# Performance work log

Measured on AMD Instinct MI355X. Metric: run time of the kernel, lower is better.

Reference implementation:

```python
import jax, jax.numpy as jnp
import numpy as np

N, E, HID, NS, NC, NCLS, NG = 100000, 1200000, 64, 16, 8, 2, 512
EPS = 1e-5


def setup_inputs() -> dict:
    key = jax.random.key(0)
    ks = jax.random.split(key, 16)
    inp = {
        "shape_id": jax.random.randint(ks[0], (N,), 0, NS),
        "colour_id": jax.random.randint(ks[1], (N,), 0, NC),
        "edge_index": jax.random.randint(ks[2], (2, E), 0, N),
        "batch": jnp.sort(jax.random.randint(ks[3], (N,), 0, NG)),
        # embeddings
        "shape_W": jax.random.normal(ks[4], (NS, HID), jnp.float32) * 0.02,
        "col_W": jax.random.normal(ks[5], (NC, HID), jnp.float32) * 0.02,
        # SAGEConv 1: lin_l (on aggregated neighbors, with bias), lin_r (on self, no bias)
        "W1l": jax.random.normal(ks[6], (HID, HID), jnp.float32) * 0.05,
        "b1": jnp.zeros((HID,), jnp.float32),
        "W1r": jax.random.normal(ks[7], (HID, HID), jnp.float32) * 0.05,
        "g1": jnp.ones((HID,), jnp.float32),
        "be1": jnp.zeros((HID,), jnp.float32),
        # SAGEConv 2
        "W2l": jax.random.normal(ks[8], (HID, HID), jnp.float32) * 0.05,
        "b2": jnp.zeros((HID,), jnp.float32),
        "W2r": jax.random.normal(ks[9], (HID, HID), jnp.float32) * 0.05,
        "g2": jnp.ones((HID,), jnp.float32),
        "be2": jnp.zeros((HID,), jnp.float32),
        # classifier
        "Wlin": jax.random.normal(ks[10], (HID, NCLS), jnp.float32) * 0.05,
        "blin": jnp.zeros((NCLS,), jnp.float32),
    }
    return inp


def _sage(x, edge_index, Wl, bl, Wr):
    # PyG SAGEConv with mean aggregation: lin_l(mean_{j in N(i)} x_j) + lin_r(x_i)
    src, dst = edge_index[0], edge_index[1]
    n = x.shape[0]
    msg_sum = jax.ops.segment_sum(x[src], dst, num_segments=n)  # [N, HID]
    cnt = jax.ops.segment_sum(jnp.ones((src.shape[0],), x.dtype), dst, num_segments=n)
    mean = msg_sum / jnp.maximum(cnt, 1.0)[:, None]
    return mean @ Wl + bl + x @ Wr


def _bn(x, gamma, beta):
    # batch-statistics normalization over node dim (training-mode BatchNorm1d)
    mu = x.mean(0)
    var = x.var(0)
    return (x - mu) * jax.lax.rsqrt(var + EPS) * gamma + beta


def reference(shape_id, colour_id, edge_index, batch,
              shape_W, col_W, W1l, b1, W1r, g1, be1,
              W2l, b2, W2r, g2, be2, Wlin, blin):
    x = shape_W[shape_id] + col_W[colour_id]                  # [N, HID]
    x = jax.nn.relu(_bn(_sage(x, edge_index, W1l, b1, W1r), g1, be1))
    # dropout(0.3) treated as identity (eval mode)
    x = jax.nn.relu(_bn(_sage(x, edge_index, W2l, b2, W2r), g2, be2))
    graph_x = jax.ops.segment_sum(x, batch, num_segments=NG)  # global_add_pool
    return graph_x @ Wlin + blin                              # [NG, NCLS]
```

## Files before the change

kernel.cpp:

```cpp
#include <hip/hip_runtime.h>
#include <stdint.h>

#define N_NODES 100000
#define N_EDGES 1200000
#define HID 64
#define NGRAPH 512
#define NCLS 2
#define BN_EPS 1e-5f

#define NTILES (N_NODES / 16)
#define NBLK_G2 782

#define BKT_SH 10
#define BKT_NODES 1024
#define NB 98
#define BKT_CAP 16000
#define EB_PER_BLK 4096
#define NBLK_E 293

typedef __attribute__((ext_vector_type(8))) short short8;
typedef __attribute__((ext_vector_type(4))) float f32x4;

__device__ inline float bf2f(uint32_t hi16) {
    uint32_t u = hi16 << 16;
    return __builtin_bit_cast(float, u);
}
__device__ inline uint32_t f2bf_rtn(float f) {
    uint32_t u = __builtin_bit_cast(uint32_t, f);
    return (u + 0x7FFFu + ((u >> 16) & 1u)) >> 16;
}

__global__ void k_code(const int* __restrict__ sid, const int* __restrict__ cid,
                       unsigned char* __restrict__ code8) {
    int i = blockIdx.x * blockDim.x + threadIdx.x;
    if (i < N_NODES) code8[i] = (unsigned char)(sid[i] | (cid[i] << 4));
}

__global__ __launch_bounds__(256) void k_tab(const float* __restrict__ sW,
                                             const float* __restrict__ cW,
                                             const float* __restrict__ W1l,
                                             const float* __restrict__ W1r,
                                             const float* __restrict__ b1,
                                             float* __restrict__ TsL,
                                             ushort* __restrict__ tblR) {
    int gid = blockIdx.x * 256 + threadIdx.x;
    if (gid < 24 * 64) {
        int row = gid >> 6, d = gid & 63;
        const float* e = (row < 16) ? &sW[row * 64] : &cW[(row - 16) * 64];
        float acc = 0.f;
        #pragma unroll 8
        for (int k = 0; k < 64; ++k) acc += e[k] * W1l[k * 64 + d];
        TsL[gid] = acc;
    } else if (gid < 24 * 64 + 128 * 64) {
        int r = gid - 24 * 64;
        int c = r >> 6, d = r & 63;
        int s = c & 15, cl = c >> 4;
        float acc = b1[d];
        #pragma unroll 8
        for (int k = 0; k < 64; ++k)
            acc += (sW[s * 64 + k] + cW[cl * 64 + k]) * W1r[k * 64 + d];
        tblR[r] = (ushort)f2bf_rtn(acc);
    }
}

__global__ __launch_bounds__(256) void k_bucket(const int* __restrict__ src,
                                                const int* __restrict__ dst,
                                                const unsigned char* __restrict__ code8,
                                                int* __restrict__ bucket_cnt,
                                                uint64_t* __restrict__ staged) {
    __shared__ int h[NB];
    __shared__ int cur[NB];
    int tid = threadIdx.x;
    if (tid < NB) h[tid] = 0;
    __syncthreads();
    uint64_t pk[16];
    int bk[16];
    int base = blockIdx.x * EB_PER_BLK;
    #pragma unroll
    for (int i = 0; i < 16; ++i) {
        int e = base + i * 256 + tid;
        if (e < N_EDGES) {
            int s = src[e], d = dst[e];
            int c = code8[s];
            bk[i] = d >> BKT_SH;
            pk[i] = ((uint64_t)c << 27) | ((uint64_t)(uint32_t)s << 10)
                  | (uint64_t)(d & (BKT_NODES - 1));
            atomicAdd(&h[bk[i]], 1);
        } else {
            bk[i] = -1;
        }
    }
    __syncthreads();
    if (tid < NB) cur[tid] = (h[tid] > 0) ? atomicAdd(&bucket_cnt[tid], h[tid]) : 0;
    __syncthreads();
    #pragma unroll
    for (int i = 0; i < 16; ++i) {
        if (bk[i] >= 0) {
            int slot = atomicAdd(&cur[bk[i]], 1);
            staged[(size_t)bk[i] * BKT_CAP + slot] = pk[i];
        }
    }
}

__global__ __launch_bounds__(128) void k_bscan(const int* __restrict__ bucket_cnt,
                                               int* __restrict__ bucket_off,
                                               int* __restrict__ row_ptr) {
    __shared__ int sh[128];
    int t = threadIdx.x;
    int v = (t < NB) ? bucket_cnt[t] : 0;
    sh[t] = v;
    __syncthreads();
    #pragma unroll
    for (int off = 1; off < 128; off <<= 1) {
        int cur = sh[t];
        int u = (t >= off) ? sh[t - off] : 0;
        __syncthreads();
        sh[t] = cur + u;
        __syncthreads();
    }
    if (t < NB) bucket_off[t] = sh[t] - v;
    if (t == 0) {
        bucket_off[NB] = N_EDGES;
        row_ptr[N_NODES] = N_EDGES;
    }
}

__global__ __launch_bounds__(256) void k_place(const uint64_t* __restrict__ staged,
                                               const int* __restrict__ bucket_off,
                                               const unsigned char* __restrict__ code8,
                                               const float* __restrict__ TsL,
                                               const ushort* __restrict__ tblR,
                                               int* __restrict__ row_ptr,
                                               int* __restrict__ csr_src,
                                               ushort* __restrict__ h1b,
                                               float* __restrict__ sums,
                                               float* __restrict__ sumsq) {
    __shared__ int hist[BKT_NODES];
    __shared__ int cursor[BKT_NODES];
    __shared__ int part[256];
    __shared__ int cnt24[BKT_NODES * 12];
    __shared__ float lsum[4][64];
    __shared__ float lsq[4][64];
    int b = blockIdx.x;
    int tid = threadIdx.x;
    int lane = tid & 63, wv = tid >> 6;
    int cc = tid & 15;
    int nodes0 = b << BKT_SH;
    int nn = min(BKT_NODES, N_NODES - nodes0);
    int ebeg = bucket_off[b];
    int cntb = bucket_off[b + 1] - ebeg;
    const uint64_t* st = &staged[(size_t)b * BKT_CAP];

    f32x4 trow[24];
    #pragma unroll
    for (int s = 0; s < 24; ++s)
        trow[s] = *(const f32x4*)&TsL[s * 64 + cc * 4];

    #pragma unroll
    for (int j = 0; j < 4; ++j) hist[tid * 4 + j] = 0;
    for (int j = tid; j < BKT_NODES * 12; j += 256) cnt24[j] = 0;
    __syncthreads();
    for (int e = tid; e < cntb; e += 256)
        atomicAdd(&hist[(int)(st[e] & (BKT_NODES - 1))], 1);
    __syncthreads();
    int c0 = hist[tid * 4 + 0], c1 = hist[tid * 4 + 1];
    int c2 = hist[tid * 4 + 2], c3 = hist[tid * 4 + 3];
    int s = c0 + c1 + c2 + c3;
    part[tid] = s;
    __syncthreads();
    #pragma unroll
    for (int off = 1; off < 256; off <<= 1) {
        int curv = part[tid];
        int u = (tid >= off) ? part[tid - off] : 0;
        __syncthreads();
        part[tid] = curv + u;
        __syncthreads();
    }
    int basev = ebeg + part[tid] - s;
    int e0 = basev, e1 = e0 + c0, e2 = e1 + c1, e3 = e2 + c2;
    cursor[tid * 4 + 0] = e0; cursor[tid * 4 + 1] = e1;
    cursor[tid * 4 + 2] = e2; cursor[tid * 4 + 3] = e3;
    #pragma unroll
    for (int j = 0; j < 4; ++j) {
        int i = tid * 4 + j;
        if (i < nn) row_ptr[nodes0 + i] = cursor[i];
    }
    __syncthreads();
    for (int e = tid; e < cntb; e += 256) {
        uint64_t pk = st[e];
        int nl = (int)(pk & (BKT_NODES - 1));
        int slot = atomicAdd(&cursor[nl], 1);
        csr_src[slot] = (int)((pk >> 10) & 0x1FFFFu);
        int c = (int)(pk >> 27);
        int sb = c & 15, cb = c >> 4;
        atomicAdd(&cnt24[nl * 12 + (sb >> 1)], 1 << ((sb & 1) * 16));
        atomicAdd(&cnt24[nl * 12 + 8 + (cb >> 1)], 1 << ((cb & 1) * 16));
    }
    __syncthreads();

    float sv0 = 0, sv1 = 0, sv2 = 0, sv3 = 0;
    float qv0 = 0, qv1 = 0, qv2 = 0, qv3 = 0;
    int nrow = tid >> 4;
    for (int it = 0; it < 64; ++it) {
        int nl = it * 16 + nrow;
        if (nl >= nn) continue;
        int node = nodes0 + nl;
        int cw[12];
        *(uint4*)&cw[0] = *(const uint4*)&cnt24[nl * 12];
        *(uint4*)&cw[4] = *(const uint4*)&cnt24[nl * 12 + 4];
        *(uint4*)&cw[8] = *(const uint4*)&cnt24[nl * 12 + 8];
        int deg = hist[nl];
        float a0 = 0, a1 = 0, a2 = 0, a3 = 0;
        #pragma unroll
        for (int ss = 0; ss < 24; ++ss) {
            int j = (ss < 16) ? (ss >> 1) : (8 + ((ss - 16) >> 1));
            float w = (float)((cw[j] >> ((ss & 1) * 16)) & 0xFFFF);
            a0 += w * trow[ss].x; a1 += w * trow[ss].y;
            a2 += w * trow[ss].z; a3 += w * trow[ss].w;
        }
        float inv = 1.f / (float)max(deg, 1);
        int ci = code8[node];
        uint2 trv = *(const uint2*)&tblR[ci * 64 + cc * 4];
        float h0 = fmaf(a0, inv, bf2f(trv.x & 0xFFFFu));
        float h1 = fmaf(a1, inv, bf2f(trv.x >> 16));
        float h2 = fmaf(a2, inv, bf2f(trv.y & 0xFFFFu));
        float h3 = fmaf(a3, inv, bf2f(trv.y >> 16));
        uint2 o;
        o.x = f2bf_rtn(h0) | (f2bf_rtn(h1) << 16);
        o.y = f2bf_rtn(h2) | (f2bf_rtn(h3) << 16);
        *(uint2*)&h1b[(size_t)node * HID + cc * 4] = o;
        sv0 += h0; qv0 += h0 * h0;
        sv1 += h1; qv1 += h1 * h1;
        sv2 += h2; qv2 += h2 * h2;
        sv3 += h3; qv3 += h3 * h3;
    }
    sv0 += __shfl_xor(sv0, 16); sv0 += __shfl_xor(sv0, 32);
    sv1 += __shfl_xor(sv1, 16); sv1 += __shfl_xor(sv1, 32);
    sv2 += __shfl_xor(sv2, 16); sv2 += __shfl_xor(sv2, 32);
    sv3 += __shfl_xor(sv3, 16); sv3 += __shfl_xor(sv3, 32);
    qv0 += __shfl_xor(qv0, 16); qv0 += __shfl_xor(qv0, 32);
    qv1 += __shfl_xor(qv1, 16); qv1 += __shfl_xor(qv1, 32);
    qv2 += __shfl_xor(qv2, 16); qv2 += __shfl_xor(qv2, 32);
    qv3 += __shfl_xor(qv3, 16); qv3 += __shfl_xor(qv3, 32);
    if ((lane >> 4) == 0) {
        lsum[wv][cc * 4 + 0] = sv0; lsum[wv][cc * 4 + 1] = sv1;
        lsum[wv][cc * 4 + 2] = sv2; lsum[wv][cc * 4 + 3] = sv3;
        lsq[wv][cc * 4 + 0] = qv0; lsq[wv][cc * 4 + 1] = qv1;
        lsq[wv][cc * 4 + 2] = qv2; lsq[wv][cc * 4 + 3] = qv3;
    }
    __syncthreads();
    if (wv == 0) {
        int d = lane;
        float S = lsum[0][d] + lsum[1][d] + lsum[2][d] + lsum[3][d];
        float Q = lsq[0][d] + lsq[1][d] + lsq[2][d] + lsq[3][d];
        atomicAdd(&sums[d], S);
        atomicAdd(&sumsq[d], Q);
    }
}

__global__ void k_bn_params(const float* __restrict__ sums, const float* __restrict__ sumsq,
                            const float* __restrict__ g, const float* __restrict__ be,
                            float* __restrict__ scale, float* __restrict__ shift) {
    int d = threadIdx.x;
    if (d >= HID) return;
    float mu  = sums[d] * (1.f / N_NODES);
    float var = sumsq[d] * (1.f / N_NODES) - mu * mu;
    float sc  = g[d] * rsqrtf(var + BN_EPS);
    scale[d] = sc;
    shift[d] = be[d] - mu * sc;
}

__global__ __launch_bounds__(256) void k_gather2(
    const ushort* __restrict__ h1b, const int* __restrict__ row_ptr,
    const int* __restrict__ csr_src,
    const float* __restrict__ scale, const float* __restrict__ shift,
    ushort* __restrict__ meanb) {
    int c = blockIdx.x;
    int x = c & 7, m = c >> 3;
    int blk = x + 8 * (m >> 3);
    if (blk >= NBLK_G2) return;
    int chunk16 = 8 * blk + (m & 7);
    if (chunk16 >= NTILES) return;
    int lane = threadIdx.x & 63, wv = threadIdx.x >> 6;
    int g = lane >> 3, cc = lane & 7;
    float4 sc0 = *(const float4*)&scale[cc * 8];
    float4 sc1 = *(const float4*)&scale[cc * 8 + 4];
    float4 sh0 = *(const float4*)&shift[cc * 8];
    float4 sh1 = *(const float4*)&shift[cc * 8 + 4];
    const uint4* x4 = (const uint4*)h1b;
    uint4* mb4 = (uint4*)meanb;
    for (int n = 0; n < 4; ++n) {
        int node = chunk16 * 16 + wv * 4 + n;
        int beg = row_ptr[node], end = row_ptr[node + 1];
        int deg = end - beg;
        float a0 = 0, a1 = 0, a2 = 0, a3 = 0, a4 = 0, a5 = 0, a6 = 0, a7 = 0;
        float b0 = 0, b1 = 0, b2 = 0, b3 = 0, b4 = 0, b5 = 0, b6 = 0, b7 = 0;
        int iters = (deg + 15) >> 4;
        for (int it = 0; it < iters; ++it) {
            int ea = beg + it * 16 + g;
            int eb = ea + 8;
            if (ea < end) {
                int sn = csr_src[ea];
                uint4 u = x4[(size_t)sn * 8 + cc];
                a0 += fmaxf(fmaf(bf2f(u.x & 0xFFFFu), sc0.x, sh0.x), 0.f);
                a1 += fmaxf(fmaf(bf2f(u.x >> 16),     sc0.y, sh0.y), 0.f);
                a2 += fmaxf(fmaf(bf2f(u.y & 0xFFFFu), sc0.z, sh0.z), 0.f);
                a3 += fmaxf(fmaf(bf2f(u.y >> 16),     sc0.w, sh0.w), 0.f);
                a4 += fmaxf(fmaf(bf2f(u.z & 0xFFFFu), sc1.x, sh1.x), 0.f);
                a5 += fmaxf(fmaf(bf2f(u.z >> 16),     sc1.y, sh1.y), 0.f);
                a6 += fmaxf(fmaf(bf2f(u.w & 0xFFFFu), sc1.z, sh1.z), 0.f);
                a7 += fmaxf(fmaf(bf2f(u.w >> 16),     sc1.w, sh1.w), 0.f);
            }
            if (eb < end) {
                int sn = csr_src[eb];
                uint4 u = x4[(size_t)sn * 8 + cc];
                b0 += fmaxf(fmaf(bf2f(u.x & 0xFFFFu), sc0.x, sh0.x), 0.f);
                b1 += fmaxf(fmaf(bf2f(u.x >> 16),     sc0.y, sh0.y), 0.f);
                b2 += fmaxf(fmaf(bf2f(u.y & 0xFFFFu), sc0.z, sh0.z), 0.f);
                b3 += fmaxf(fmaf(bf2f(u.y >> 16),     sc0.w, sh0.w), 0.f);
                b4 += fmaxf(fmaf(bf2f(u.z & 0xFFFFu), sc1.x, sh1.x), 0.f);
                b5 += fmaxf(fmaf(bf2f(u.z >> 16),     sc1.y, sh1.y), 0.f);
                b6 += fmaxf(fmaf(bf2f(u.w & 0xFFFFu), sc1.z, sh1.z), 0.f);
                b7 += fmaxf(fmaf(bf2f(u.w >> 16),     sc1.w, sh1.w), 0.f);
            }
        }
        a0 += b0; a1 += b1; a2 += b2; a3 += b3;
        a4 += b4; a5 += b5; a6 += b6; a7 += b7;
        #pragma unroll
        for (int off = 8; off < 64; off <<= 1) {
            a0 += __shfl_xor(a0, off); a1 += __shfl_xor(a1, off);
            a2 += __shfl_xor(a2, off); a3 += __shfl_xor(a3, off);
            a4 += __shfl_xor(a4, off); a5 += __shfl_xor(a5, off);
            a6 += __shfl_xor(a6, off); a7 += __shfl_xor(a7, off);
        }
        if (lane < 8) {
            float inv = 1.f / (float)max(deg, 1);
            uint4 o;
            o.x = f2bf_rtn(a0 * inv) | (f2bf_rtn(a1 * inv) << 16);
            o.y = f2bf_rtn(a2 * inv) | (f2bf_rtn(a3 * inv) << 16);
            o.z = f2bf_rtn(a4 * inv) | (f2bf_rtn(a5 * inv) << 16);
            o.w = f2bf_rtn(a6 * inv) | (f2bf_rtn(a7 * inv) << 16);
            mb4[(size_t)node * 8 + lane] = o;
        }
    }
}

__global__ void k_wpack(const float* __restrict__ Wl, const float* __restrict__ Wr,
                        ushort* __restrict__ wpk) {
    int gid = blockIdx.x * blockDim.x + threadIdx.x;
    if (gid >= 1024) return;
    int tile = gid >> 6;
    int lane = gid & 63;
    int nt = tile >> 2, kt = tile & 3;
    #pragma unroll
    for (int j = 0; j < 8; ++j) {
        int k = kt * 32 + (lane >> 4) * 8 + j;
        int n = nt * 16 + (lane & 15);
        float v = (k < 64) ? Wl[k * HID + n] : Wr[(k - 64) * HID + n];
        wpk[(size_t)(tile * 64 + lane) * 8 + j] = (ushort)f2bf_rtn(v);
    }
}

__global__ __launch_bounds__(256) void k_gemm2(
    const ushort* __restrict__ meanb, const ushort* __restrict__ h1b,
    const ushort* __restrict__ wpk, const float* __restrict__ bias,
    const float* __restrict__ scale, const float* __restrict__ shift,
    ushort* __restrict__ hout, float* __restrict__ sums, float* __restrict__ sumsq) {
    __shared__ float lsum[4][64];
    __shared__ float lsq[4][64];
    int lane = threadIdx.x & 63;
    int wv = threadIdx.x >> 6;
    int r16 = lane & 15;
    int grp = lane >> 4;
    short8 bfrag[4][4];
    const short8* wp = (const short8*)wpk;
    #pragma unroll
    for (int nt = 0; nt < 4; ++nt)
        #pragma unroll
        for (int kt = 0; kt < 4; ++kt)
            bfrag[nt][kt] = wp[(nt * 4 + kt) * 64 + lane];
    float bcol[4];
    #pragma unroll
    for (int nt = 0; nt < 4; ++nt) bcol[nt] = bias[nt * 16 + r16];
    float4 scA0 = *(const float4*)&scale[grp * 8];
    float4 scA1 = *(const float4*)&scale[grp * 8 + 4];
    float4 shA0 = *(const float4*)&shift[grp * 8];
    float4 shA1 = *(const float4*)&shift[grp * 8 + 4];
    float4 scB0 = *(const float4*)&scale[32 + grp * 8];
    float4 scB1 = *(const float4*)&scale[32 + grp * 8 + 4];
    float4 shB0 = *(const float4*)&shift[32 + grp * 8];
    float4 shB1 = *(const float4*)&shift[32 + grp * 8 + 4];

    int tbase = (blockIdx.x * 4 + wv) * 2;
    int t0 = tbase, t1 = tbase + 1;
    bool v0 = t0 < NTILES, v1 = t1 < NTILES;

    short8 am0[2], am1[2];
    uint2 u0[4], u1[4];
    if (v0) {
        int node = t0 * 16 + r16;
        const short8* mrow = (const short8*)(meanb + (size_t)node * HID);
        am0[0] = mrow[grp];
        am0[1] = mrow[4 + grp];
        const uint2* s2 = (const uint2*)(h1b + (size_t)node * HID);
        u0[0] = s2[grp * 2]; u0[1] = s2[grp * 2 + 1];
        u0[2] = s2[8 + grp * 2]; u0[3] = s2[9 + grp * 2];
    }
    if (v1) {
        int node = t1 * 16 + r16;
        const short8* mrow = (const short8*)(meanb + (size_t)node * HID);
        am1[0] = mrow[grp];
        am1[1] = mrow[4 + grp];
        const uint2* s2 = (const uint2*)(h1b + (size_t)node * HID);
        u1[0] = s2[grp * 2]; u1[1] = s2[grp * 2 + 1];
        u1[2] = s2[8 + grp * 2]; u1[3] = s2[9 + grp * 2];
    }

    float sv[4] = {0.f, 0.f, 0.f, 0.f}, qv[4] = {0.f, 0.f, 0.f, 0.f};

    #pragma unroll
    for (int j = 0; j < 2; ++j) {
        bool valid = j == 0 ? v0 : v1;
        if (!valid) continue;
        int tile = j == 0 ? t0 : t1;
        short8* amp = j == 0 ? am0 : am1;
        uint2* up = j == 0 ? u0 : u1;
        short8 a2v, a3v;
        a2v[0] = (short)f2bf_rtn(fmaxf(fmaf(bf2f(up[0].x & 0xFFFFu), scA0.x, shA0.x), 0.f));
        a2v[1] = (short)f2bf_rtn(fmaxf(fmaf(bf2f(up[0].x >> 16),     scA0.y, shA0.y), 0.f));
        a2v[2] = (short)f2bf_rtn(fmaxf(fmaf(bf2f(up[0].y & 0xFFFFu), scA0.z, shA0.z), 0.f));
        a2v[3] = (short)f2bf_rtn(fmaxf(fmaf(bf2f(up[0].y >> 16),     scA0.w, shA0.w), 0.f));
        a2v[4] = (short)f2bf_rtn(fmaxf(fmaf(bf2f(up[1].x & 0xFFFFu), scA1.x, shA1.x), 0.f));
        a2v[5] = (short)f2bf_rtn(fmaxf(fmaf(bf2f(up[1].x >> 16),     scA1.y, shA1.y), 0.f));
        a2v[6] = (short)f2bf_rtn(fmaxf(fmaf(bf2f(up[1].y & 0xFFFFu), scA1.z, shA1.z), 0.f));
        a2v[7] = (short)f2bf_rtn(fmaxf(fmaf(bf2f(up[1].y >> 16),     scA1.w, shA1.w), 0.f));
        a3v[0] = (short)f2bf_rtn(fmaxf(fmaf(bf2f(up[2].x & 0xFFFFu), scB0.x, shB0.x), 0.f));
        a3v[1] = (short)f2bf_rtn(fmaxf(fmaf(bf2f(up[2].x >> 16),     scB0.y, shB0.y), 0.f));
        a3v[2] = (short)f2bf_rtn(fmaxf(fmaf(bf2f(up[2].y & 0xFFFFu), scB0.z, shB0.z), 0.f));
        a3v[3] = (short)f2bf_rtn(fmaxf(fmaf(bf2f(up[2].y >> 16),     scB0.w, shB0.w), 0.f));
        a3v[4] = (short)f2bf_rtn(fmaxf(fmaf(bf2f(up[3].x & 0xFFFFu), scB1.x, shB1.x), 0.f));
        a3v[5] = (short)f2bf_rtn(fmaxf(fmaf(bf2f(up[3].x >> 16),     scB1.y, shB1.y), 0.f));
        a3v[6] = (short)f2bf_rtn(fmaxf(fmaf(bf2f(up[3].y & 0xFFFFu), scB1.z, shB1.z), 0.f));
        a3v[7] = (short)f2bf_rtn(fmaxf(fmaf(bf2f(up[3].y >> 16),     scB1.w, shB1.w), 0.f));
        short8 a[4];
        a[0] = amp[0];
        a[1] = amp[1];
        a[2] = a2v;
        a[3] = a3v;
        f32x4 acc[4];
        #pragma unroll
        for (int nt = 0; nt < 4; ++nt) acc[nt] = (f32x4){0.f, 0.f, 0.f, 0.f};
        #pragma unroll
        for (int nt = 0; nt < 4; ++nt)
            #pragma unroll
            for (int kt = 0; kt < 4; ++kt)
                acc[nt] = __builtin_amdgcn_mfma_f32_16x16x32_bf16(a[kt], bfrag[nt][kt],
                                                                  acc[nt], 0, 0, 0);
        #pragma unroll
        for (int nt = 0; nt < 4; ++nt) {
            #pragma unroll
            for (int r = 0; r < 4; ++r) {
                float hv = acc[nt][r] + bcol[nt];
                int rrow = tile * 16 + grp * 4 + r;
                hout[(size_t)rrow * HID + nt * 16 + r16] = (ushort)f2bf_rtn(hv);
                sv[nt] += hv;
                qv[nt] += hv * hv;
            }
        }
    }
    #pragma unroll
    for (int nt = 0; nt < 4; ++nt) {
        float v = sv[nt];
        v += __shfl_xor(v, 16); v += __shfl_xor(v, 32);
        float q = qv[nt];
        q += __shfl_xor(q, 16); q += __shfl_xor(q, 32);
        if (grp == 0) {
            lsum[wv][nt * 16 + r16] = v;
            lsq[wv][nt * 16 + r16] = q;
        }
    }
    __syncthreads();
    if (wv == 0) {
        int d = lane;
        float S = lsum[0][d] + lsum[1][d] + lsum[2][d] + lsum[3][d];
        float Q = lsq[0][d] + lsq[1][d] + lsq[2][d] + lsq[3][d];
        atomicAdd(&sums[d], S);
        atomicAdd(&sumsq[d], Q);
    }
}

__global__ __launch_bounds__(256) void k_pool(const ushort* __restrict__ h,
                                              const int* __restrict__ batch,
                                              const float* __restrict__ scale,
                                              const float* __restrict__ shift,
                                              float* __restrict__ graph_x) {
    int wv = threadIdx.x >> 6, d = threadIdx.x & 63;
    float sc = scale[d], sh = shift[d];
    const int NCHUNK = 4096;
    int cidx = blockIdx.x * 4 + wv;
    int chunk = (N_NODES + NCHUNK - 1) / NCHUNK;
    int a = cidx * chunk;
    int b = min(a + chunk, N_NODES);
    if (a >= b) return;
    int cur = batch[a];
    float acc = 0.f;
    for (int i = a; i < b; ++i) {
        int g = batch[i];
        if (g != cur) {
            atomicAdd(&graph_x[cur * HID + d], acc);
            acc = 0.f;
            cur = g;
        }
        float v = bf2f((uint32_t)h[(size_t)i * HID + d]);
        acc += fmaxf(fmaf(v, sc, sh), 0.f);
    }
    atomicAdd(&graph_x[cur * HID + d], acc);
}

__global__ void k_cls(const float* __restrict__ graph_x, const float* __restrict__ Wlin,
                      const float* __restrict__ blin, float* __restrict__ out) {
    int idx = blockIdx.x * blockDim.x + threadIdx.x;
    if (idx >= NGRAPH * NCLS) return;
    int g = idx / NCLS, c = idx % NCLS;
    float acc = blin[c];
    #pragma unroll
    for (int k = 0; k < HID; ++k) acc += graph_x[g * HID + k] * Wlin[k * NCLS + c];
    out[idx] = acc;
}

extern "C" void kernel_launch(void* const* d_in, const int* in_sizes, int n_in,
                              void* d_out, int out_size, void* d_ws, size_t ws_size,
                              hipStream_t stream) {
    const int*   sid   = (const int*)d_in[0];
    const int*   cid   = (const int*)d_in[1];
    const int*   esrc  = (const int*)d_in[2];
    const int*   edst  = esrc + N_EDGES;
    const int*   batch = (const int*)d_in[3];
    const float* sW    = (const float*)d_in[4];
    const float* cW    = (const float*)d_in[5];
    const float* W1l   = (const float*)d_in[6];
    const float* b1    = (const float*)d_in[7];
    const float* W1r   = (const float*)d_in[8];
    const float* g1    = (const float*)d_in[9];
    const float* be1   = (const float*)d_in[10];
    const float* W2l   = (const float*)d_in[11];
    const float* b2    = (const float*)d_in[12];
    const float* W2r   = (const float*)d_in[13];
    const float* g2    = (const float*)d_in[14];
    const float* be2   = (const float*)d_in[15];
    const float* Wlin  = (const float*)d_in[16];
    const float* blin  = (const float*)d_in[17];
    float* out = (float*)d_out;

    const size_t FEAT = (size_t)N_NODES * HID;
    ushort* scratch = (ushort*)d_ws;
    ushort* h1b   = scratch + FEAT;
    ushort* h2b   = h1b + FEAT;
    ushort* wpk2  = h2b + FEAT;
    ushort* tblR  = wpk2 + 8192;
    float* TsL    = (float*)(tblR + 8192);
    float* fp     = TsL + 24 * 64;
    float* sums1  = fp;            float* sumsq1 = sums1 + HID;
    float* sums2  = sumsq1 + HID;  float* sumsq2 = sums2 + HID;
    float* scale1 = sumsq2 + HID;  float* shift1 = scale1 + HID;
    float* scale2 = shift1 + HID;  float* shift2 = scale2 + HID;
    float* graph_x = shift2 + HID;
    int* row_ptr  = (int*)(graph_x + (size_t)NGRAPH * HID);
    int* csr_src  = row_ptr + N_NODES + 1;
    int* bucket_cnt = csr_src + N_EDGES;
    int* bucket_off = bucket_cnt + NB;
    unsigned char* code8 = (unsigned char*)(bucket_off + NB + 1);
    uint64_t* staged = (uint64_t*)scratch;
    ushort* meanb = scratch;

    hipMemsetAsync(bucket_cnt, 0, NB * sizeof(int), stream);
    hipMemsetAsync(sums1, 0, 4 * HID * sizeof(float), stream);
    hipMemsetAsync(graph_x, 0, (size_t)NGRAPH * HID * sizeof(float), stream);

    k_code<<<(N_NODES + 255) / 256, 256, 0, stream>>>(sid, cid, code8);
    k_tab<<<38, 256, 0, stream>>>(sW, cW, W1l, W1r, b1, TsL, tblR);
    k_wpack<<<4, 256, 0, stream>>>(W2l, W2r, wpk2);

    k_bucket<<<NBLK_E, 256, 0, stream>>>(esrc, edst, code8, bucket_cnt, staged);
    k_bscan<<<1, 128, 0, stream>>>(bucket_cnt, bucket_off, row_ptr);
    k_place<<<NB, 256, 0, stream>>>(staged, bucket_off, code8, TsL, tblR,
                                    row_ptr, csr_src, h1b, sums1, sumsq1);
    k_bn_params<<<1, 64, 0, stream>>>(sums1, sumsq1, g1, be1, scale1, shift1);

    k_gather2<<<8 * 784, 256, 0, stream>>>(h1b, row_ptr, csr_src, scale1, shift1, meanb);
    k_gemm2<<<NBLK_G2, 256, 0, stream>>>(meanb, h1b, wpk2, b2, scale1, shift1,
                                         h2b, sums2, sumsq2);
    k_bn_params<<<1, 64, 0, stream>>>(sums2, sumsq2, g2, be2, scale2, shift2);

    k_pool<<<1024, 256, 0, stream>>>(h2b, batch, scale2, shift2, graph_x);
    k_cls<<<(NGRAPH * NCLS + 255) / 256, 256, 0, stream>>>(graph_x, Wlin, blin, out);
}
```

Baseline: 191.3 us.

## Shrink CSR buckets to 256 nodes and pack staged edges into 32 bits

Cuts the destination bucket size from 1024 to 256 nodes, so the CSR placement kernel runs 391 blocks instead of 98 and fills more of the GPU. Staged edge records shrink from 64-bit to 32-bit packing (code, source and local destination), halving staging traffic. The per-block scan and loops are adjusted to one node per thread. Bucket capacity drops to 4080 per bucket, which risks overflow if the destination distribution is skewed, and the bucket kernel now does more global atomics on the per-bucket counters.

```diff
diff --git a/kernel.cpp b/kernel.cpp
--- a/kernel.cpp
+++ b/kernel.cpp
@@ -11,10 +11,10 @@
 #define NTILES (N_NODES / 16)
 #define NBLK_G2 782
 
-#define BKT_SH 10
-#define BKT_NODES 1024
-#define NB 98
-#define BKT_CAP 16000
+#define BKT_SH 8
+#define BKT_NODES 256
+#define NB 391
+#define BKT_CAP 4080
 #define EB_PER_BLK 4096
 #define NBLK_E 293
 
@@ -67,13 +67,13 @@
                                                 const int* __restrict__ dst,
                                                 const unsigned char* __restrict__ code8,
                                                 int* __restrict__ bucket_cnt,
-                                                uint64_t* __restrict__ staged) {
+                                                uint32_t* __restrict__ staged) {
     __shared__ int h[NB];
     __shared__ int cur[NB];
     int tid = threadIdx.x;
-    if (tid < NB) h[tid] = 0;
-    __syncthreads();
-    uint64_t pk[16];
+    for (int j = tid; j < NB; j += 256) h[j] = 0;
+    __syncthreads();
+    uint32_t pk[16];
     int bk[16];
     int base = blockIdx.x * EB_PER_BLK;
     #pragma unroll
@@ -83,15 +83,16 @@
             int s = src[e], d = dst[e];
             int c = code8[s];
             bk[i] = d >> BKT_SH;
-            pk[i] = ((uint64_t)c << 27) | ((uint64_t)(uint32_t)s << 10)
-                  | (uint64_t)(d & (BKT_NODES - 1));
+            pk[i] = ((uint32_t)c << 25) | ((uint32_t)s << 8)
+                  | (uint32_t)(d & (BKT_NODES - 1));
             atomicAdd(&h[bk[i]], 1);
         } else {
             bk[i] = -1;
         }
     }
     __syncthreads();
-    if (tid < NB) cur[tid] = (h[tid] > 0) ? atomicAdd(&bucket_cnt[tid], h[tid]) : 0;
+    for (int j = tid; j < NB; j += 256)
+        cur[j] = (h[j] > 0) ? atomicAdd(&bucket_cnt[j], h[j]) : 0;
     __syncthreads();
     #pragma unroll
     for (int i = 0; i < 16; ++i) {
@@ -102,16 +103,16 @@
     }
 }
 
-__global__ __launch_bounds__(128) void k_bscan(const int* __restrict__ bucket_cnt,
+__global__ __launch_bounds__(512) void k_bscan(const int* __restrict__ bucket_cnt,
                                                int* __restrict__ bucket_off,
                                                int* __restrict__ row_ptr) {
-    __shared__ int sh[128];
+    __shared__ int sh[512];
     int t = threadIdx.x;
     int v = (t < NB) ? bucket_cnt[t] : 0;
     sh[t] = v;
     __syncthreads();
     #pragma unroll
-    for (int off = 1; off < 128; off <<= 1) {
+    for (int off = 1; off < 512; off <<= 1) {
         int cur = sh[t];
         int u = (t >= off) ? sh[t - off] : 0;
         __syncthreads();
@@ -125,7 +126,7 @@
     }
 }
 
-__global__ __launch_bounds__(256) void k_place(const uint64_t* __restrict__ staged,
+__global__ __launch_bounds__(256) void k_place(const uint32_t* __restrict__ staged,
                                                const int* __restrict__ bucket_off,
                                                const unsigned char* __restrict__ code8,
                                                const float* __restrict__ TsL,
@@ -149,24 +150,22 @@
     int nn = min(BKT_NODES, N_NODES - nodes0);
     int ebeg = bucket_off[b];
     int cntb = bucket_off[b + 1] - ebeg;
-    const uint64_t* st = &staged[(size_t)b * BKT_CAP];
+    const uint32_t* st = &staged[(size_t)b * BKT_CAP];
 
     f32x4 trow[24];
     #pragma unroll
     for (int s = 0; s < 24; ++s)
         trow[s] = *(const f32x4*)&TsL[s * 64 + cc * 4];
 
-    #pragma unroll
-    for (int j = 0; j < 4; ++j) hist[tid * 4 + j] = 0;
-    for (int j = tid; j < BKT_NODES * 12; j += 256) cnt24[j] = 0;
+    hist[tid] = 0;
+    #pragma unroll
+    for (int j = 0; j < 12; ++j) cnt24[tid * 12 + j] = 0;
     __syncthreads();
     for (int e = tid; e < cntb; e += 256)
         atomicAdd(&hist[(int)(st[e] & (BKT_NODES - 1))], 1);
     __syncthreads();
-    int c0 = hist[tid * 4 + 0], c1 = hist[tid * 4 + 1];
-    int c2 = hist[tid * 4 + 2], c3 = hist[tid * 4 + 3];
-    int s = c0 + c1 + c2 + c3;
-    part[tid] = s;
+    int myc = hist[tid];
+    part[tid] = myc;
     __syncthreads();
     #pragma unroll
     for (int off = 1; off < 256; off <<= 1) {
@@ -176,22 +175,16 @@
         part[tid] = curv + u;
         __syncthreads();
     }
-    int basev = ebeg + part[tid] - s;
-    int e0 = basev, e1 = e0 + c0, e2 = e1 + c1, e3 = e2 + c2;
-    cursor[tid * 4 + 0] = e0; cursor[tid * 4 + 1] = e1;
-    cursor[tid * 4 + 2] = e2; cursor[tid * 4 + 3] = e3;
-    #pragma unroll
-    for (int j = 0; j < 4; ++j) {
-        int i = tid * 4 + j;
-        if (i < nn) row_ptr[nodes0 + i] = cursor[i];
-    }
+    int ex = ebeg + part[tid] - myc;
+    cursor[tid] = ex;
+    if (tid < nn) row_ptr[nodes0 + tid] = ex;
     __syncthreads();
     for (int e = tid; e < cntb; e += 256) {
-        uint64_t pk = st[e];
+        uint32_t pk = st[e];
         int nl = (int)(pk & (BKT_NODES - 1));
         int slot = atomicAdd(&cursor[nl], 1);
-        csr_src[slot] = (int)((pk >> 10) & 0x1FFFFu);
-        int c = (int)(pk >> 27);
+        csr_src[slot] = (int)((pk >> 8) & 0x1FFFFu);
+        int c = (int)(pk >> 25);
         int sb = c & 15, cb = c >> 4;
         atomicAdd(&cnt24[nl * 12 + (sb >> 1)], 1 << ((sb & 1) * 16));
         atomicAdd(&cnt24[nl * 12 + 8 + (cb >> 1)], 1 << ((cb & 1) * 16));
@@ -201,7 +194,7 @@
     float sv0 = 0, sv1 = 0, sv2 = 0, sv3 = 0;
     float qv0 = 0, qv1 = 0, qv2 = 0, qv3 = 0;
     int nrow = tid >> 4;
-    for (int it = 0; it < 64; ++it) {
+    for (int it = 0; it < 16; ++it) {
         int nl = it * 16 + nrow;
         if (nl >= nn) continue;
         int node = nodes0 + nl;
@@ -570,7 +563,7 @@
     int* bucket_cnt = csr_src + N_EDGES;
     int* bucket_off = bucket_cnt + NB;
     unsigned char* code8 = (unsigned char*)(bucket_off + NB + 1);
-    uint64_t* staged = (uint64_t*)scratch;
+    uint32_t* staged = (uint32_t*)scratch;
     ushort* meanb = scratch;
 
     hipMemsetAsync(bucket_cnt, 0, NB * sizeof(int), stream);
@@ -582,7 +575,7 @@
     k_wpack<<<4, 256, 0, stream>>>(W2l, W2r, wpk2);
 
     k_bucket<<<NBLK_E, 256, 0, stream>>>(esrc, edst, code8, bucket_cnt, staged);
-    k_bscan<<<1, 128, 0, stream>>>(bucket_cnt, bucket_off, row_ptr);
+    k_bscan<<<1, 512, 0, stream>>>(bucket_cnt, bucket_off, row_ptr);
     k_place<<<NB, 256, 0, stream>>>(staged, bucket_off, code8, TsL, tblR,
                                     row_ptr, csr_src, h1b, sums1, sumsq1);
     k_bn_params<<<1, 64, 0, stream>>>(sums1, sumsq1, g1, be1, scale1, shift1);
```

Result: faster. 167.2 us (-12.6%).
